# Kernel tuning notes

Measured on AMD Instinct MI355X. Metric: run time of the kernel, lower is better.

## Reference

```python
import jax, jax.numpy as jnp
import numpy as np

EMBED_DIM = 512
KERNEL = 17


def setup_inputs() -> dict:
    key = jax.random.key(0)
    ks = jax.random.split(key, 5)
    B, L, C = 2, 8192, EMBED_DIM
    s = C ** -0.5
    x = jax.random.normal(ks[0], (B, L, C), dtype=jnp.float32)
    # weights stored as (in, out); equivalent to torch Linear weight.T
    w_qkv = jax.random.normal(ks[1], (C, 3 * C), dtype=jnp.float32) * s
    w_width = jax.random.normal(ks[2], (C, 1), dtype=jnp.float32) * s
    b_width = jax.random.normal(ks[3], (1,), dtype=jnp.float32) * 0.01
    w_out = jax.random.normal(ks[4], (C, C), dtype=jnp.float32) * s
    return {"x": x, "w_qkv": w_qkv, "w_width": w_width, "b_width": b_width, "w_out": w_out}


def reference(x, w_qkv, w_width, b_width, w_out):
    B, L, C = x.shape
    K = KERNEL
    half_k = K // 2
    scale = C ** -0.5

    qkv = x @ w_qkv                      # [B,L,3C]
    q, k, v = jnp.split(qkv, 3, axis=-1)

    # learned soft window width in [1, K]
    width = jax.nn.sigmoid(x @ w_width + b_width) * (K - 1) + 1.0   # [B,L,1]

    # sliding windows of k/v: pad along L then gather K-sized windows
    k_pad = jnp.pad(k, ((0, 0), (half_k, half_k), (0, 0)))
    v_pad = jnp.pad(v, ((0, 0), (half_k, half_k), (0, 0)))
    idx = jnp.arange(L)[:, None] + jnp.arange(K)[None, :]           # [L,K]
    k_win = k_pad[:, idx]                # [B,L,K,C]
    v_win = v_pad[:, idx]                # [B,L,K,C]

    scores = jnp.einsum('blc,blkc->blk', q, k_win) * scale          # [B,L,K]

    rel_pos = jnp.abs(jnp.arange(K, dtype=jnp.float32) - half_k)    # [K]
    soft_mask = jax.nn.sigmoid((width - rel_pos) * 5.0)             # [B,L,K]
    scores = scores - (1.0 - soft_mask) * 10000.0

    attn = jax.nn.softmax(scores, axis=-1)
    out = jnp.einsum('blk,blkc->blc', attn, v_win)                  # [B,L,C]
    return (out + v) @ w_out
```

## Files before the change

kernel.cpp:

```cpp
#include <hip/hip_runtime.h>

typedef unsigned short u16;
typedef unsigned int   u32;
typedef __attribute__((ext_vector_type(8))) short          shortx8;
typedef __attribute__((ext_vector_type(8))) unsigned short ushortx8;
typedef __attribute__((ext_vector_type(4))) float          floatx4;

#define AS1 __attribute__((address_space(1)))
#define AS3 __attribute__((address_space(3)))

#define SEG 8208
#define LV  16416

__device__ __forceinline__ float b2f(u16 v) {
  return __uint_as_float(((u32)v) << 16);
}
__device__ __forceinline__ u16 f2b(float f) {
  u32 u = __float_as_uint(f);
  u += 0x7FFF + ((u >> 16) & 1);
  return (u16)(u >> 16);
}
__device__ __forceinline__ void cp16(const void* g, void* l) {
  __builtin_amdgcn_global_load_lds((AS1 u32*)g, (AS3 u32*)l, 16, 0, 0);
}

__global__ __launch_bounds__(256)
void prep(const float* __restrict__ x, const float* __restrict__ w_width,
          const float* __restrict__ b_width, const float* __restrict__ w_qkv,
          const float* __restrict__ w_out, u16* __restrict__ xb,
          float* __restrict__ width, u16* __restrict__ BtAll,
          u16* __restrict__ woutT, u16* __restrict__ Vt) {
  __shared__ alignas(16) u16 shb[17408];
  __shared__ u16 tile[32][33];
  const int b = blockIdx.x;
  if (b < 16) {
    const int t    = b;
    const int row0 = (t >> 2) * 128;
    const int col0 = (t & 3) * 128;
    const int tid  = threadIdx.x;
    const int lane = tid & 63;
    const int wave = tid >> 6;
    const int quad = lane >> 4;
    const int lr   = lane & 15;
    const int wr   = (wave >> 1) * 64;
    const int wc   = (wave & 1) * 64;
    u16* As = shb;
    u16* Bs = shb + 8192;

    floatx4 acc[4][4];
#pragma unroll
    for (int i = 0; i < 4; ++i)
#pragma unroll
      for (int j = 0; j < 4; ++j) acc[i][j] = (floatx4)0.0f;

    int srow[4], scol[4];
#pragma unroll
    for (int p = 0; p < 4; ++p) {
      int c = p * 256 + tid;
      srow[p] = c >> 3;
      scol[p] = ((c & 7) ^ (srow[p] & 7)) * 8;
    }
    const int swz = lr & 7;

    for (int k0 = 0; k0 < 512; k0 += 64) {
#pragma unroll
      for (int p = 0; p < 4; ++p) {
        const float* ga = w_qkv + (size_t)(row0 + srow[p]) * 1536 + k0 + scol[p];
        floatx4 a0 = *(const floatx4*)ga;
        floatx4 a1 = *(const floatx4*)(ga + 4);
        ushortx8 o;
#pragma unroll
        for (int j = 0; j < 4; ++j) { o[j] = f2b(a0[j]); o[4 + j] = f2b(a1[j]); }
        *(ushortx8*)&As[(p * 256 + tid) * 8] = o;
      }
#pragma unroll
      for (int p = 0; p < 4; ++p) {
        const float* gb = w_qkv + (size_t)(col0 + srow[p]) * 1536 + 512 + k0 + scol[p];
        floatx4 b0 = *(const floatx4*)gb;
        floatx4 b1 = *(const floatx4*)(gb + 4);
        ushortx8 o;
#pragma unroll
        for (int j = 0; j < 4; ++j) { o[j] = f2b(b0[j]); o[4 + j] = f2b(b1[j]); }
        *(ushortx8*)&Bs[(p * 256 + tid) * 8] = o;
      }
      __syncthreads();
#pragma unroll
      for (int ks = 0; ks < 2; ++ks) {
        shortx8 af[4], bf[4];
#pragma unroll
        for (int mi = 0; mi < 4; ++mi)
          af[mi] = *(const shortx8*)
              &As[((wr + mi * 16 + lr) * 8 + ((ks * 4 + quad) ^ swz)) * 8];
#pragma unroll
        for (int ni = 0; ni < 4; ++ni)
          bf[ni] = *(const shortx8*)
              &Bs[((wc + ni * 16 + lr) * 8 + ((ks * 4 + quad) ^ swz)) * 8];
#pragma unroll
        for (int mi = 0; mi < 4; ++mi)
#pragma unroll
          for (int ni = 0; ni < 4; ++ni)
            acc[mi][ni] = __builtin_amdgcn_mfma_f32_16x16x32_bf16(
                af[mi], bf[ni], acc[mi][ni], 0, 0, 0);
      }
      __syncthreads();
    }
#pragma unroll
    for (int mi = 0; mi < 4; ++mi)
#pragma unroll
      for (int ni = 0; ni < 4; ++ni)
#pragma unroll
        for (int r = 0; r < 4; ++r)
          shb[(wc + ni * 16 + lr) * 136 + wr + mi * 16 + quad * 4 + r] =
              f2b(acc[mi][ni][r]);
    __syncthreads();
    const int rr = tid >> 4, cc = (tid & 15) * 8;
#pragma unroll
    for (int it = 0; it < 8; ++it) {
      int chl = it * 16 + rr;
      *(ushortx8*)(BtAll + (size_t)(col0 + chl) * 512 + row0 + cc) =
          *(const ushortx8*)&shb[chl * 136 + cc];
    }
  } else if (b < 4112) {
    const int lane = threadIdx.x & 63;
    const int row  = (b - 16) * 4 + (threadIdx.x >> 6);
    const float* xp = x + (size_t)row * 512 + lane * 8;
    floatx4 v0 = *(const floatx4*)xp;
    floatx4 v1 = *(const floatx4*)(xp + 4);
    floatx4 w0 = *(const floatx4*)(w_width + lane * 8);
    floatx4 w1 = *(const floatx4*)(w_width + lane * 8 + 4);
    float s = 0.f;
    ushortx8 o;
#pragma unroll
    for (int j = 0; j < 4; ++j) {
      s += v0[j] * w0[j] + v1[j] * w1[j];
      o[j] = f2b(v0[j]); o[4 + j] = f2b(v1[j]);
    }
    *(ushortx8*)(xb + (size_t)row * 512 + lane * 8) = o;
#pragma unroll
    for (int m = 32; m >= 1; m >>= 1) s += __shfl_xor(s, m, 64);
    if (lane == 0)
      width[row] = 16.f / (1.f + __expf(-(s + b_width[0]))) + 1.f;
  } else if (b < 4624) {
    const float* in = (b < 4368) ? w_qkv : w_out;
    const int C  = (b < 4368) ? 1536 : 512;
    const int t  = (b < 4368) ? (b - 4112) : (b - 4368);
    const int cbo = (b < 4368) ? 1024 : 0;
    u16* out = (b < 4368) ? (BtAll + 512 * 512) : woutT;
    const int cb = cbo + (t & 15) * 32;
    const int rb = (t >> 4) * 32;
    const int tx = threadIdx.x & 31;
    const int ty = threadIdx.x >> 5;
#pragma unroll
    for (int i = 0; i < 32; i += 8)
      tile[ty + i][tx] = f2b(in[(size_t)(rb + ty + i) * C + cb + tx]);
    __syncthreads();
#pragma unroll
    for (int i = 0; i < 32; i += 8)
      out[(size_t)(cb - cbo + ty + i) * 512 + rb + tx] = tile[tx][ty + i];
  } else {
    const int idx = (b - 4624) * 256 + threadIdx.x;
    const int ch = idx >> 5;
    const int k  = idx & 31;
    const int seg = k >> 4;
    const int j   = k & 15;
    const int col = seg * SEG + (j < 8 ? j : 8192 + j);
    Vt[(size_t)ch * LV + col] = 0;
  }
}

__global__ __launch_bounds__(256, 3)
void gemm_qv(const u16* __restrict__ A, const u16* __restrict__ Bt,
             u16* __restrict__ Qb, u16* __restrict__ Vt) {
  const int K = 512;
  __shared__ alignas(16) u16 lds[17408];
  u16* As = lds;
  u16* Bs = lds + 8192;
  const int tid  = threadIdx.x;
  const int lane = tid & 63;
  const int wave = tid >> 6;
  const int quad = lane >> 4;
  const int lr   = lane & 15;
  const int row0 = blockIdx.x * 128;
  const int col0 = blockIdx.y * 128;
  const int wr   = (wave >> 1) * 64;
  const int wc   = (wave & 1) * 64;

  floatx4 acc[4][4];
#pragma unroll
  for (int i = 0; i < 4; ++i)
#pragma unroll
    for (int j = 0; j < 4; ++j) acc[i][j] = (floatx4)0.0f;

  int srow[4], scol[4];
#pragma unroll
  for (int p = 0; p < 4; ++p) {
    int c = p * 256 + tid;
    srow[p] = c >> 3;
    scol[p] = ((c & 7) ^ (srow[p] & 7)) * 8;
  }
  const int swz = lr & 7;

  for (int k0 = 0; k0 < K; k0 += 64) {
#pragma unroll
    for (int p = 0; p < 4; ++p)
      cp16(A + (size_t)(row0 + srow[p]) * K + k0 + scol[p], &As[(p * 256 + tid) * 8]);
#pragma unroll
    for (int p = 0; p < 4; ++p)
      cp16(Bt + (size_t)(col0 + srow[p]) * K + k0 + scol[p], &Bs[(p * 256 + tid) * 8]);
    __syncthreads();

#pragma unroll
    for (int ks = 0; ks < 2; ++ks) {
      shortx8 af[4], bf[4];
#pragma unroll
      for (int mi = 0; mi < 4; ++mi)
        af[mi] = *(const shortx8*)
            &As[((wr + mi * 16 + lr) * 8 + ((ks * 4 + quad) ^ swz)) * 8];
#pragma unroll
      for (int ni = 0; ni < 4; ++ni)
        bf[ni] = *(const shortx8*)
            &Bs[((wc + ni * 16 + lr) * 8 + ((ks * 4 + quad) ^ swz)) * 8];
#pragma unroll
      for (int mi = 0; mi < 4; ++mi)
#pragma unroll
        for (int ni = 0; ni < 4; ++ni)
          acc[mi][ni] = __builtin_amdgcn_mfma_f32_16x16x32_bf16(
              af[mi], bf[ni], acc[mi][ni], 0, 0, 0);
    }
    __syncthreads();
  }

  if (col0 < 512) {
    const int cb = col0;
#pragma unroll
    for (int mi = 0; mi < 4; ++mi)
#pragma unroll
      for (int ni = 0; ni < 4; ++ni)
#pragma unroll
        for (int r = 0; r < 4; ++r)
          lds[(wr + mi * 16 + quad * 4 + r) * 136 + wc + ni * 16 + lr] =
              f2b(acc[mi][ni][r]);
    __syncthreads();
    const int rr = tid >> 4, cc = (tid & 15) * 8;
#pragma unroll
    for (int it = 0; it < 8; ++it) {
      int row = it * 16 + rr;
      *(ushortx8*)(Qb + (size_t)(row0 + row) * 512 + cb + cc) =
          *(const ushortx8*)&lds[row * 136 + cc];
    }
  } else {
    const int cb = col0 - 512;
    const int bb = row0 >> 13, pib0 = row0 & 8191;
#pragma unroll
    for (int mi = 0; mi < 4; ++mi)
#pragma unroll
      for (int ni = 0; ni < 4; ++ni)
#pragma unroll
        for (int r = 0; r < 4; ++r)
          lds[(wc + ni * 16 + lr) * 136 + wr + mi * 16 + quad * 4 + r] =
              f2b(acc[mi][ni][r]);
    __syncthreads();
    const int rr = tid >> 4, cc = (tid & 15) * 8;
#pragma unroll
    for (int it = 0; it < 8; ++it) {
      int chl = it * 16 + rr;
      ushortx8 v = *(const ushortx8*)&lds[chl * 136 + cc];
      *(ushortx8*)(Vt + (size_t)(cb + chl) * LV + (size_t)bb * SEG + 8 + pib0 + cc) = v;
    }
  }
}

__global__ __launch_bounds__(256, 1)
void attn_fused(const u16* __restrict__ Q, const u16* __restrict__ Kx,
                const u16* __restrict__ Vt, const float* __restrict__ width,
                const u16* __restrict__ woutT, float* __restrict__ Out) {
  __shared__ alignas(16) u16 Osw[64 * 256];
  __shared__ alignas(16) u16 P[4][16][32];
  const int tid  = threadIdx.x;
  const int lane = tid & 63;
  const int wave = tid >> 6;
  const int quad = lane >> 4;
  const int lr   = lane & 15;
  const int p0   = blockIdx.x * 64;
  const int pw   = p0 + wave * 16;
  const int pibw = pw & 8191;
  const int bb   = pw >> 13;
  const size_t cb0 = (size_t)bb * SEG + pibw;

  shortx8 vfA[16];
#pragma unroll
  for (int ctl = 0; ctl < 16; ++ctl)
    vfA[ctl] = *(const shortx8*)(Vt + (size_t)(ctl * 16 + lr) * LV +
                                 cb0 + quad * 8);

  floatx4 s0 = (floatx4)0.0f, s1 = (floatx4)0.0f;
#pragma unroll 4
  for (int s = 0; s < 16; ++s) {
    const int k0 = s * 32 + quad * 8;
    shortx8 af = *(const shortx8*)(Q  + (size_t)(pw + lr) * 512 + k0);
    shortx8 f0 = *(const shortx8*)(Kx + (ptrdiff_t)(pw - 8 + lr) * 512 + k0);
    shortx8 f1 = *(const shortx8*)(Kx + (ptrdiff_t)(pw + 8 + lr) * 512 + k0);
    s0 = __builtin_amdgcn_mfma_f32_16x16x32_bf16(af, f0, s0, 0, 0, 0);
    s1 = __builtin_amdgcn_mfma_f32_16x16x32_bf16(af, f1, s1, 0, 0, 0);
  }

  {
    const float scale = 0.044194173824159216f;
    floatx4 wv = *(const floatx4*)(width + pw + quad * 4);
#pragma unroll
    for (int r = 0; r < 4; ++r) {
      const int row = quad * 4 + r;
      const int d0  = lr - row;
      const int d1  = d0 + 16;
      const int jb0 = pibw + lr - 8;
      const int jb1 = jb0 + 16;
      float rel0 = fabsf((float)(d0 - 8));
      float rel1 = fabsf((float)(d1 - 8));
      float mk0 = 1.f / (1.f + __expf(-5.f * (wv[r] - rel0)));
      float mk1 = 1.f / (1.f + __expf(-5.f * (wv[r] - rel1)));
      float val0 = (d0 >= 0)
          ? (((unsigned)jb0 < 8192u ? s0[r] * scale : 0.f) - (1.f - mk0) * 10000.f)
          : -1e30f;
      float val1 = (d1 <= 16)
          ? (((unsigned)jb1 < 8192u ? s1[r] * scale : 0.f) - (1.f - mk1) * 10000.f)
          : -1e30f;
      float mx = fmaxf(val0, val1);
#pragma unroll
      for (int m = 8; m >= 1; m >>= 1) mx = fmaxf(mx, __shfl_xor(mx, m, 64));
      float e0 = __expf(val0 - mx), e1 = __expf(val1 - mx);
      float sum = e0 + e1;
#pragma unroll
      for (int m = 8; m >= 1; m >>= 1) sum += __shfl_xor(sum, m, 64);
      const float inv = 1.f / sum;
      P[wave][row][lr]      = f2b(e0 * inv + (d0 == 8 ? 1.f : 0.f));
      P[wave][row][lr + 16] = f2b(e1 * inv + (d1 == 8 ? 1.f : 0.f));
    }
  }
  shortx8 pf = *(const shortx8*)&P[wave][lr][quad * 8];

  const int wc = wave * 128;
  floatx4 acc[4][8];
#pragma unroll
  for (int mi = 0; mi < 4; ++mi)
#pragma unroll
    for (int ni = 0; ni < 8; ++ni) acc[mi][ni] = (floatx4)0.0f;

  shortx8 vfB[16];
#pragma unroll
  for (int ctl = 0; ctl < 16; ++ctl)
    vfB[ctl] = *(const shortx8*)(Vt + (size_t)(256 + ctl * 16 + lr) * LV +
                                 cb0 + quad * 8);

#pragma unroll
  for (int ctl = 0; ctl < 16; ++ctl) {
    floatx4 o = __builtin_amdgcn_mfma_f32_16x16x32_bf16(pf, vfA[ctl],
                                                        (floatx4)0.0f, 0, 0, 0);
    const int c = ctl * 2 + (lr >> 3);
#pragma unroll
    for (int r = 0; r < 4; ++r) {
      const int row = wave * 16 + quad * 4 + r;
      Osw[row * 256 + (((c & ~7) | ((c & 7) ^ (row & 7))) << 3) + (lr & 7)] =
          f2b(o[r]);
    }
  }
  __syncthreads();

  {
    shortx8 bcur[8], bnxt[8];
#pragma unroll
    for (int ni = 0; ni < 8; ++ni)
      bcur[ni] = *(const shortx8*)(woutT + (size_t)(wc + ni * 16 + lr) * 512 +
                                   quad * 8);
    for (int ksl = 0; ksl < 8; ++ksl) {
      if (ksl < 7) {
#pragma unroll
        for (int ni = 0; ni < 8; ++ni)
          bnxt[ni] = *(const shortx8*)(woutT +
                       (size_t)(wc + ni * 16 + lr) * 512 +
                       (ksl + 1) * 32 + quad * 8);
      }
      shortx8 afr[4];
#pragma unroll
      for (int mi = 0; mi < 4; ++mi) {
        const int row = mi * 16 + lr;
        const int c = ksl * 4 + quad;
        afr[mi] = *(const shortx8*)
            &Osw[row * 256 + (((c & ~7) | ((c & 7) ^ (row & 7))) << 3)];
      }
#pragma unroll
      for (int mi = 0; mi < 4; ++mi)
#pragma unroll
        for (int ni = 0; ni < 8; ++ni)
          acc[mi][ni] = __builtin_amdgcn_mfma_f32_16x16x32_bf16(
              afr[mi], bcur[ni], acc[mi][ni], 0, 0, 0);
      if (ksl < 7) {
#pragma unroll
        for (int ni = 0; ni < 8; ++ni) bcur[ni] = bnxt[ni];
      }
    }
  }
  __syncthreads();

#pragma unroll
  for (int ctl = 0; ctl < 16; ++ctl) {
    floatx4 o = __builtin_amdgcn_mfma_f32_16x16x32_bf16(pf, vfB[ctl],
                                                        (floatx4)0.0f, 0, 0, 0);
    const int c = ctl * 2 + (lr >> 3);
#pragma unroll
    for (int r = 0; r < 4; ++r) {
      const int row = wave * 16 + quad * 4 + r;
      Osw[row * 256 + (((c & ~7) | ((c & 7) ^ (row & 7))) << 3) + (lr & 7)] =
          f2b(o[r]);
    }
  }
  __syncthreads();

  {
    shortx8 bcur[8], bnxt[8];
#pragma unroll
    for (int ni = 0; ni < 8; ++ni)
      bcur[ni] = *(const shortx8*)(woutT + (size_t)(wc + ni * 16 + lr) * 512 +
                                   256 + quad * 8);
    for (int ksl = 0; ksl < 8; ++ksl) {
      if (ksl < 7) {
#pragma unroll
        for (int ni = 0; ni < 8; ++ni)
          bnxt[ni] = *(const shortx8*)(woutT +
                       (size_t)(wc + ni * 16 + lr) * 512 +
                       256 + (ksl + 1) * 32 + quad * 8);
      }
      shortx8 afr[4];
#pragma unroll
      for (int mi = 0; mi < 4; ++mi) {
        const int row = mi * 16 + lr;
        const int c = ksl * 4 + quad;
        afr[mi] = *(const shortx8*)
            &Osw[row * 256 + (((c & ~7) | ((c & 7) ^ (row & 7))) << 3)];
      }
#pragma unroll
      for (int mi = 0; mi < 4; ++mi)
#pragma unroll
        for (int ni = 0; ni < 8; ++ni)
          acc[mi][ni] = __builtin_amdgcn_mfma_f32_16x16x32_bf16(
              afr[mi], bcur[ni], acc[mi][ni], 0, 0, 0);
      if (ksl < 7) {
#pragma unroll
        for (int ni = 0; ni < 8; ++ni) bcur[ni] = bnxt[ni];
      }
    }
  }

#pragma unroll
  for (int mi = 0; mi < 4; ++mi)
#pragma unroll
    for (int ni = 0; ni < 8; ++ni)
#pragma unroll
      for (int r = 0; r < 4; ++r)
        Out[(size_t)(p0 + mi * 16 + quad * 4 + r) * 512 + wc + ni * 16 + lr] =
            acc[mi][ni][r];
}

extern "C" void kernel_launch(void* const* d_in, const int* in_sizes, int n_in,
                              void* d_out, int out_size, void* d_ws, size_t ws_size,
                              hipStream_t stream) {
  const float* x       = (const float*)d_in[0];
  const float* w_qkv   = (const float*)d_in[1];
  const float* w_width = (const float*)d_in[2];
  const float* b_width = (const float*)d_in[3];
  const float* w_out   = (const float*)d_in[4];
  float* out = (float*)d_out;

  const int M = 16384;
  char* ws = (char*)d_ws;
  u16*   xb    = (u16*)(ws + 8192);
  u16*   Qb    = (u16*)(ws + 16793600);
  u16*   Vt    = (u16*)(ws + 33579008);
  u16*   BtAll = (u16*)(ws + 50397184);
  u16*   woutT = (u16*)(ws + 51453952);
  float* width = (float*)(ws + 51986432);

  prep<<<dim3(4688), dim3(256), 0, stream>>>(x, w_width, b_width, w_qkv, w_out,
                                             xb, width, BtAll, woutT, Vt);
  gemm_qv<<<dim3(M / 128, 8), dim3(256), 0, stream>>>(xb, BtAll, Qb, Vt);
  attn_fused<<<dim3(M / 64), dim3(256), 0, stream>>>(Qb, xb, Vt, width, woutT,
                                                     out);
}
```

Measured before the change: 153.9 us.

## Fold output projection into value weights, removing the per-row output GEMM

Uses linearity to precompute W_v·W_out (and W_k-folded matrices) in the prep kernel, so the gemm_qv kernel directly produces the projected values. The attention kernel then writes the attention-weighted sum of projected values straight to the output, which drops the second 512x512 GEMM per tile, the LDS staging buffer and its barriers. The cost is a small extra weight-weight GEMM in prep with strided w_out loads. Precision changes slightly because the folded matrix is rounded to bf16.

```diff
diff --git a/kernel.cpp b/kernel.cpp
--- a/kernel.cpp
+++ b/kernel.cpp
@@ -29,12 +29,12 @@
           const float* __restrict__ b_width, const float* __restrict__ w_qkv,
           const float* __restrict__ w_out, u16* __restrict__ xb,
           float* __restrict__ width, u16* __restrict__ BtAll,
-          u16* __restrict__ woutT, u16* __restrict__ Vt) {
+          u16* __restrict__ Vt) {
   __shared__ alignas(16) u16 shb[17408];
-  __shared__ u16 tile[32][33];
   const int b = blockIdx.x;
-  if (b < 16) {
-    const int t    = b;
+  if (b < 32) {
+    const bool isMc = (b < 16);
+    const int t    = isMc ? b : b - 16;
     const int row0 = (t >> 2) * 128;
     const int col0 = (t & 3) * 128;
     const int tid  = threadIdx.x;
@@ -65,7 +65,8 @@
     for (int k0 = 0; k0 < 512; k0 += 64) {
 #pragma unroll
       for (int p = 0; p < 4; ++p) {
-        const float* ga = w_qkv + (size_t)(row0 + srow[p]) * 1536 + k0 + scol[p];
+        const float* ga = w_qkv + (size_t)(row0 + srow[p]) * 1536 +
+                          (isMc ? 0 : 1024) + k0 + scol[p];
         floatx4 a0 = *(const floatx4*)ga;
         floatx4 a1 = *(const floatx4*)(ga + 4);
         ushortx8 o;
@@ -75,12 +76,19 @@
       }
 #pragma unroll
       for (int p = 0; p < 4; ++p) {
-        const float* gb = w_qkv + (size_t)(col0 + srow[p]) * 1536 + 512 + k0 + scol[p];
-        floatx4 b0 = *(const floatx4*)gb;
-        floatx4 b1 = *(const floatx4*)(gb + 4);
         ushortx8 o;
-#pragma unroll
-        for (int j = 0; j < 4; ++j) { o[j] = f2b(b0[j]); o[4 + j] = f2b(b1[j]); }
+        if (isMc) {
+          const float* gb = w_qkv + (size_t)(col0 + srow[p]) * 1536 + 512 +
+                            k0 + scol[p];
+          floatx4 b0 = *(const floatx4*)gb;
+          floatx4 b1 = *(const floatx4*)(gb + 4);
+#pragma unroll
+          for (int j = 0; j < 4; ++j) { o[j] = f2b(b0[j]); o[4 + j] = f2b(b1[j]); }
+        } else {
+          const float* gb = w_out + (size_t)(k0 + scol[p]) * 512 + col0 + srow[p];
+#pragma unroll
+          for (int j = 0; j < 8; ++j) o[j] = f2b(gb[(size_t)j * 512]);
+        }
         *(ushortx8*)&Bs[(p * 256 + tid) * 8] = o;
       }
       __syncthreads();
@@ -104,6 +112,7 @@
       }
       __syncthreads();
     }
+    u16* outp = BtAll + (isMc ? 0 : (size_t)512 * 512);
 #pragma unroll
     for (int mi = 0; mi < 4; ++mi)
 #pragma unroll
@@ -117,12 +126,12 @@
 #pragma unroll
     for (int it = 0; it < 8; ++it) {
       int chl = it * 16 + rr;
-      *(ushortx8*)(BtAll + (size_t)(col0 + chl) * 512 + row0 + cc) =
+      *(ushortx8*)(outp + (size_t)(col0 + chl) * 512 + row0 + cc) =
           *(const ushortx8*)&shb[chl * 136 + cc];
     }
-  } else if (b < 4112) {
+  } else if (b < 4128) {
     const int lane = threadIdx.x & 63;
-    const int row  = (b - 16) * 4 + (threadIdx.x >> 6);
+    const int row  = (b - 32) * 4 + (threadIdx.x >> 6);
     const float* xp = x + (size_t)row * 512 + lane * 8;
     floatx4 v0 = *(const floatx4*)xp;
     floatx4 v1 = *(const floatx4*)(xp + 4);
@@ -140,25 +149,8 @@
     for (int m = 32; m >= 1; m >>= 1) s += __shfl_xor(s, m, 64);
     if (lane == 0)
       width[row] = 16.f / (1.f + __expf(-(s + b_width[0]))) + 1.f;
-  } else if (b < 4624) {
-    const float* in = (b < 4368) ? w_qkv : w_out;
-    const int C  = (b < 4368) ? 1536 : 512;
-    const int t  = (b < 4368) ? (b - 4112) : (b - 4368);
-    const int cbo = (b < 4368) ? 1024 : 0;
-    u16* out = (b < 4368) ? (BtAll + 512 * 512) : woutT;
-    const int cb = cbo + (t & 15) * 32;
-    const int rb = (t >> 4) * 32;
-    const int tx = threadIdx.x & 31;
-    const int ty = threadIdx.x >> 5;
-#pragma unroll
-    for (int i = 0; i < 32; i += 8)
-      tile[ty + i][tx] = f2b(in[(size_t)(rb + ty + i) * C + cb + tx]);
-    __syncthreads();
-#pragma unroll
-    for (int i = 0; i < 32; i += 8)
-      out[(size_t)(cb - cbo + ty + i) * 512 + rb + tx] = tile[tx][ty + i];
   } else {
-    const int idx = (b - 4624) * 256 + threadIdx.x;
+    const int idx = (b - 4128) * 256 + threadIdx.x;
     const int ch = idx >> 5;
     const int k  = idx & 31;
     const int seg = k >> 4;
@@ -273,8 +265,7 @@
 __global__ __launch_bounds__(256, 1)
 void attn_fused(const u16* __restrict__ Q, const u16* __restrict__ Kx,
                 const u16* __restrict__ Vt, const float* __restrict__ width,
-                const u16* __restrict__ woutT, float* __restrict__ Out) {
-  __shared__ alignas(16) u16 Osw[64 * 256];
+                float* __restrict__ Out) {
   __shared__ alignas(16) u16 P[4][16][32];
   const int tid  = threadIdx.x;
   const int lane = tid & 63;
@@ -303,6 +294,12 @@
     s0 = __builtin_amdgcn_mfma_f32_16x16x32_bf16(af, f0, s0, 0, 0, 0);
     s1 = __builtin_amdgcn_mfma_f32_16x16x32_bf16(af, f1, s1, 0, 0, 0);
   }
+
+  shortx8 vfB[16];
+#pragma unroll
+  for (int ctl = 0; ctl < 16; ++ctl)
+    vfB[ctl] = *(const shortx8*)(Vt + (size_t)(256 + ctl * 16 + lr) * LV +
+                                 cb0 + quad * 8);
 
   {
     const float scale = 0.044194173824159216f;
@@ -338,126 +335,22 @@
   }
   shortx8 pf = *(const shortx8*)&P[wave][lr][quad * 8];
 
-  const int wc = wave * 128;
-  floatx4 acc[4][8];
-#pragma unroll
-  for (int mi = 0; mi < 4; ++mi)
-#pragma unroll
-    for (int ni = 0; ni < 8; ++ni) acc[mi][ni] = (floatx4)0.0f;
-
-  shortx8 vfB[16];
-#pragma unroll
-  for (int ctl = 0; ctl < 16; ++ctl)
-    vfB[ctl] = *(const shortx8*)(Vt + (size_t)(256 + ctl * 16 + lr) * LV +
-                                 cb0 + quad * 8);
-
 #pragma unroll
   for (int ctl = 0; ctl < 16; ++ctl) {
     floatx4 o = __builtin_amdgcn_mfma_f32_16x16x32_bf16(pf, vfA[ctl],
                                                         (floatx4)0.0f, 0, 0, 0);
-    const int c = ctl * 2 + (lr >> 3);
-#pragma unroll
-    for (int r = 0; r < 4; ++r) {
-      const int row = wave * 16 + quad * 4 + r;
-      Osw[row * 256 + (((c & ~7) | ((c & 7) ^ (row & 7))) << 3) + (lr & 7)] =
-          f2b(o[r]);
-    }
-  }
-  __syncthreads();
-
-  {
-    shortx8 bcur[8], bnxt[8];
-#pragma unroll
-    for (int ni = 0; ni < 8; ++ni)
-      bcur[ni] = *(const shortx8*)(woutT + (size_t)(wc + ni * 16 + lr) * 512 +
-                                   quad * 8);
-    for (int ksl = 0; ksl < 8; ++ksl) {
-      if (ksl < 7) {
-#pragma unroll
-        for (int ni = 0; ni < 8; ++ni)
-          bnxt[ni] = *(const shortx8*)(woutT +
-                       (size_t)(wc + ni * 16 + lr) * 512 +
-                       (ksl + 1) * 32 + quad * 8);
-      }
-      shortx8 afr[4];
-#pragma unroll
-      for (int mi = 0; mi < 4; ++mi) {
-        const int row = mi * 16 + lr;
-        const int c = ksl * 4 + quad;
-        afr[mi] = *(const shortx8*)
-            &Osw[row * 256 + (((c & ~7) | ((c & 7) ^ (row & 7))) << 3)];
-      }
-#pragma unroll
-      for (int mi = 0; mi < 4; ++mi)
-#pragma unroll
-        for (int ni = 0; ni < 8; ++ni)
-          acc[mi][ni] = __builtin_amdgcn_mfma_f32_16x16x32_bf16(
-              afr[mi], bcur[ni], acc[mi][ni], 0, 0, 0);
-      if (ksl < 7) {
-#pragma unroll
-        for (int ni = 0; ni < 8; ++ni) bcur[ni] = bnxt[ni];
-      }
-    }
-  }
-  __syncthreads();
-
+#pragma unroll
+    for (int r = 0; r < 4; ++r)
+      Out[(size_t)(pw + quad * 4 + r) * 512 + ctl * 16 + lr] = o[r];
+  }
 #pragma unroll
   for (int ctl = 0; ctl < 16; ++ctl) {
     floatx4 o = __builtin_amdgcn_mfma_f32_16x16x32_bf16(pf, vfB[ctl],
                                                         (floatx4)0.0f, 0, 0, 0);
-    const int c = ctl * 2 + (lr >> 3);
-#pragma unroll
-    for (int r = 0; r < 4; ++r) {
-      const int row = wave * 16 + quad * 4 + r;
-      Osw[row * 256 + (((c & ~7) | ((c & 7) ^ (row & 7))) << 3) + (lr & 7)] =
-          f2b(o[r]);
-    }
-  }
-  __syncthreads();
-
-  {
-    shortx8 bcur[8], bnxt[8];
-#pragma unroll
-    for (int ni = 0; ni < 8; ++ni)
-      bcur[ni] = *(const shortx8*)(woutT + (size_t)(wc + ni * 16 + lr) * 512 +
-                                   256 + quad * 8);
-    for (int ksl = 0; ksl < 8; ++ksl) {
-      if (ksl < 7) {
-#pragma unroll
-        for (int ni = 0; ni < 8; ++ni)
-          bnxt[ni] = *(const shortx8*)(woutT +
-                       (size_t)(wc + ni * 16 + lr) * 512 +
-                       256 + (ksl + 1) * 32 + quad * 8);
-      }
-      shortx8 afr[4];
-#pragma unroll
-      for (int mi = 0; mi < 4; ++mi) {
-        const int row = mi * 16 + lr;
-        const int c = ksl * 4 + quad;
-        afr[mi] = *(const shortx8*)
-            &Osw[row * 256 + (((c & ~7) | ((c & 7) ^ (row & 7))) << 3)];
-      }
-#pragma unroll
-      for (int mi = 0; mi < 4; ++mi)
-#pragma unroll
-        for (int ni = 0; ni < 8; ++ni)
-          acc[mi][ni] = __builtin_amdgcn_mfma_f32_16x16x32_bf16(
-              afr[mi], bcur[ni], acc[mi][ni], 0, 0, 0);
-      if (ksl < 7) {
-#pragma unroll
-        for (int ni = 0; ni < 8; ++ni) bcur[ni] = bnxt[ni];
-      }
-    }
-  }
-
-#pragma unroll
-  for (int mi = 0; mi < 4; ++mi)
-#pragma unroll
-    for (int ni = 0; ni < 8; ++ni)
-#pragma unroll
-      for (int r = 0; r < 4; ++r)
-        Out[(size_t)(p0 + mi * 16 + quad * 4 + r) * 512 + wc + ni * 16 + lr] =
-            acc[mi][ni][r];
+#pragma unroll
+    for (int r = 0; r < 4; ++r)
+      Out[(size_t)(pw + quad * 4 + r) * 512 + 256 + ctl * 16 + lr] = o[r];
+  }
 }
 
 extern "C" void kernel_launch(void* const* d_in, const int* in_sizes, int n_in,
@@ -476,12 +369,10 @@
   u16*   Qb    = (u16*)(ws + 16793600);
   u16*   Vt    = (u16*)(ws + 33579008);
   u16*   BtAll = (u16*)(ws + 50397184);
-  u16*   woutT = (u16*)(ws + 51453952);
-  float* width = (float*)(ws + 51986432);
-
-  prep<<<dim3(4688), dim3(256), 0, stream>>>(x, w_width, b_width, w_qkv, w_out,
-                                             xb, width, BtAll, woutT, Vt);
+  float* width = (float*)(ws + 51445760);
+
+  prep<<<dim3(4192), dim3(256), 0, stream>>>(x, w_width, b_width, w_qkv, w_out,
+                                             xb, width, BtAll, Vt);
   gemm_qv<<<dim3(M / 128, 8), dim3(256), 0, stream>>>(xb, BtAll, Qb, Vt);
-  attn_fused<<<dim3(M / 64), dim3(256), 0, stream>>>(Qb, xb, Vt, width, woutT,
-                                                     out);
-}
+  attn_fused<<<dim3(M / 64), dim3(256), 0, stream>>>(Qb, xb, Vt, width, out);
+}
```

New measurement: 165.0 us. 7.2% more time.
